# Kernel optimization log

Measured on AMD Instinct MI355X. Metric: run time of the kernel, lower is better.

## Reference

```python
import jax, jax.numpy as jnp
import numpy as np
import math

D_MODEL = 256
D_HEAD = 64
N_LEVELS = 2
N_HEADS = 8
N_POINTS = 4
SHAPES = [(100, 176), (50, 88)]  # (H, W) per level -> Len_in = 22000


def setup_inputs() -> dict:
    key = jax.random.key(0)
    ks = jax.random.split(key, 8)
    N, Lq = 2, 22000
    Len_in = sum(h * w for h, w in SHAPES)
    query = jax.random.normal(ks[0], (N, Lq, D_MODEL), jnp.float32)
    input_flatten = jax.random.normal(ks[1], (N, Len_in, D_MODEL), jnp.float32)
    input_spatial_shapes = jnp.array(SHAPES, jnp.int32)
    input_level_start_index = jnp.array([0, SHAPES[0][0] * SHAPES[0][1]], jnp.int32)
    # reference points in pixel units (original divides them by offset_normalizer)
    norm = jnp.array([[w, h] for (h, w) in SHAPES], jnp.float32)  # [L,2] as (x=W, y=H)
    reference_points = jax.random.uniform(ks[2], (N, Lq, N_LEVELS, 2), jnp.float32) * norm[None, None]
    xav = lambda k, shp: jax.random.normal(k, shp, jnp.float32) * math.sqrt(2.0 / (shp[0] + shp[1]))
    Wv = xav(ks[3], (D_MODEL, N_HEADS * D_HEAD))
    bv = jnp.zeros((N_HEADS * D_HEAD,), jnp.float32)
    Woff = jax.random.normal(ks[4], (D_MODEL, N_HEADS * N_LEVELS * N_POINTS * 2), jnp.float32) * 0.01
    # grid-init bias exactly as in _reset_parameters
    thetas = jnp.arange(N_HEADS, dtype=jnp.float32) * (2.0 * math.pi / N_HEADS)
    grid = jnp.stack([jnp.cos(thetas), jnp.sin(thetas)], -1)
    grid = grid / jnp.max(jnp.abs(grid), -1, keepdims=True)
    grid = jnp.tile(grid[:, None, None, :], (1, N_LEVELS, N_POINTS, 1))
    grid = grid * jnp.arange(1, N_POINTS + 1, dtype=jnp.float32)[None, None, :, None]
    boff = grid.reshape(-1)
    Wattn = jax.random.normal(ks[5], (D_MODEL, N_HEADS * N_LEVELS * N_POINTS), jnp.float32) * 0.01
    battn = jnp.zeros((N_HEADS * N_LEVELS * N_POINTS,), jnp.float32)
    Wo = xav(ks[6], (N_HEADS * D_HEAD, D_MODEL))
    bo = jnp.zeros((D_MODEL,), jnp.float32)
    return dict(query=query, reference_points=reference_points, input_flatten=input_flatten,
                Wv=Wv, bv=bv, Woff=Woff, boff=boff, Wattn=Wattn, battn=battn, Wo=Wo, bo=bo,
                input_spatial_shapes=input_spatial_shapes,
                input_level_start_index=input_level_start_index)


def ms_deform_core(value, sampling_locations, attention_weights, shapes_np):
    # value: [N, Len_in, H, D]; sampling_locations: [N, Lq, H, L, P, 2] in [0,1]
    # attention_weights: [N, Lq, H, L, P]
    N, _, Hh_, D = value.shape
    Lq = sampling_locations.shape[1]
    P = sampling_locations.shape[4]
    out = jnp.zeros((N, Lq, Hh_, D), value.dtype)
    start = 0
    for lvl, (Hl, Wl) in enumerate(shapes_np):
        Hl, Wl = int(Hl), int(Wl)
        v = value[:, start:start + Hl * Wl]  # [N, Hl*Wl, H, D]
        start += Hl * Wl
        loc = sampling_locations[:, :, :, lvl]  # [N, Lq, H, P, 2]
        # grid_sample align_corners=False convention
        x = loc[..., 0] * Wl - 0.5
        y = loc[..., 1] * Hl - 0.5
        x0 = jnp.floor(x); y0 = jnp.floor(y)
        fx = x - x0; fy = y - y0
        x0i = x0.astype(jnp.int32); y0i = y0.astype(jnp.int32)
        acc = jnp.zeros((N, Lq, P, Hh_, D), value.dtype)
        for dx, dy, w in ((0, 0, (1 - fx) * (1 - fy)), (1, 0, fx * (1 - fy)),
                          (0, 1, (1 - fx) * fy), (1, 1, fx * fy)):
            xi = x0i + dx; yi = y0i + dy
            valid = (xi >= 0) & (xi < Wl) & (yi >= 0) & (yi < Hl)
            idx = jnp.clip(yi, 0, Hl - 1) * Wl + jnp.clip(xi, 0, Wl - 1)  # [N, Lq, H, P]
            idx_t = idx.transpose(0, 1, 3, 2).reshape(N, Lq * P, Hh_, 1)
            g = jnp.take_along_axis(v, idx_t, axis=1).reshape(N, Lq, P, Hh_, D)
            wz = jnp.where(valid, w, 0.0)  # zero padding outside
            acc = acc + g * wz.transpose(0, 1, 3, 2)[..., None]
        out = out + jnp.einsum('nqphd,nqhp->nqhd', acc, attention_weights[:, :, :, lvl])
    return out.reshape(N, Lq, Hh_ * D)


def reference(query, reference_points, input_flatten, Wv, bv, Woff, boff, Wattn, battn, Wo, bo,
              input_spatial_shapes, input_level_start_index):
    shapes_np = np.asarray(input_spatial_shapes)
    N, Lq, _ = query.shape
    value = (input_flatten @ Wv + bv).reshape(N, -1, N_HEADS, D_HEAD)
    off = (query @ Woff + boff).reshape(N, Lq, N_HEADS, N_LEVELS, N_POINTS, 2)
    aw = jax.nn.softmax((query @ Wattn + battn).reshape(N, Lq, N_HEADS, N_LEVELS * N_POINTS), -1)
    aw = aw.reshape(N, Lq, N_HEADS, N_LEVELS, N_POINTS)
    normalizer = jnp.stack([shapes_np[:, 1], shapes_np[:, 0]], -1).astype(jnp.float32)  # [L,2] (W,H)
    loc = (reference_points[:, :, None, :, None, :] + off) / normalizer[None, None, None, :, None, :]
    out = ms_deform_core(value, loc, aw, shapes_np)
    return out @ Wo + bo
```

## Files before the change

kernel.cpp:

```cpp
#include <hip/hip_runtime.h>

#define LQ        22000
#define LEN_IN    22000
#define NB        2

typedef _Float16 half8 __attribute__((ext_vector_type(8)));
typedef _Float16 half4 __attribute__((ext_vector_type(4)));
typedef float    floatx4 __attribute__((ext_vector_type(4)));

__global__ __launch_bounds__(256) void prep_kernel(
    const float* __restrict__ Wv, const float* __restrict__ Woff,
    const float* __restrict__ Wattn, const float* __restrict__ Wo,
    const float* __restrict__ boff, const float* __restrict__ battn,
    _Float16* __restrict__ WvT, _Float16* __restrict__ WofT,
    _Float16* __restrict__ WoT, float* __restrict__ biascat)
{
    const int i = blockIdx.x * 256 + threadIdx.x;
    if (i < 131072) {
        int k = i >> 9, n = i & 511;
        WvT[n * 256 + k] = (_Float16)Wv[i];
    } else if (i < 163840) {
        int j = i - 131072; int k = j >> 7, n = j & 127;
        WofT[n * 256 + k] = (_Float16)Woff[j];
    } else if (i < 180224) {
        int j = i - 163840; int k = j >> 6, n = j & 63;
        WofT[(128 + n) * 256 + k] = (_Float16)Wattn[j];
    } else if (i < 311296) {
        int j = i - 180224; int k = j >> 8, n = j & 255;
        WoT[n * 512 + k] = (_Float16)Wo[j];
    } else if (i < 311488) {
        int j = i - 311296;
        biascat[j] = (j < 128) ? boff[j] : battn[j - 128];
    }
}

__global__ void f32_to_f16_kernel(const float* __restrict__ src,
                                  _Float16* __restrict__ dst, int n4)
{
    int i = blockIdx.x * blockDim.x + threadIdx.x;
    const int stride = gridDim.x * blockDim.x;
    for (; i < n4; i += stride) {
        float4 v = reinterpret_cast<const float4*>(src)[i];
        half4 h;
        h[0] = (_Float16)v.x; h[1] = (_Float16)v.y;
        h[2] = (_Float16)v.z; h[3] = (_Float16)v.w;
        reinterpret_cast<half4*>(dst)[i] = h;
    }
}

template<bool OUT_F16>
__global__ __launch_bounds__(256) void gemm_f16_kernel(
    const _Float16* __restrict__ A,
    const _Float16* __restrict__ BT,
    const float* __restrict__ bias,
    void* __restrict__ C,
    int M, int N, int K)
{
    __shared__ __align__(16) _Float16 sA[128][72];
    __shared__ __align__(16) _Float16 sB[64][72];

    const int t  = threadIdx.x;
    const int m0 = blockIdx.x * 128;
    const int n0 = blockIdx.y * 64;

    const int w    = t >> 6;
    const int lane = t & 63;
    const int wm   = w * 32;
    const int lrow = lane & 15;
    const int lk   = (lane >> 4) * 8;

    const int ar = t >> 1;
    const int ah = (t & 1) * 32;
    const int br = t >> 2;
    const int bs = (t & 3) * 16;

    floatx4 acc[2][4] = {};

    for (int k0 = 0; k0 < K; k0 += 64) {
        {
            int4 v0 = {0,0,0,0}, v1 = {0,0,0,0}, v2 = {0,0,0,0}, v3 = {0,0,0,0};
            const int arow = m0 + ar;
            if (arow < M) {
                const int4* src = reinterpret_cast<const int4*>(A + (size_t)arow * K + k0 + ah);
                v0 = src[0]; v1 = src[1]; v2 = src[2]; v3 = src[3];
            }
            int4* dst = reinterpret_cast<int4*>(&sA[ar][ah]);
            dst[0] = v0; dst[1] = v1; dst[2] = v2; dst[3] = v3;
        }
        {
            const int4* src = reinterpret_cast<const int4*>(BT + (size_t)(n0 + br) * K + k0 + bs);
            int4* dst = reinterpret_cast<int4*>(&sB[br][bs]);
            dst[0] = src[0]; dst[1] = src[1];
        }
        __syncthreads();

        #pragma unroll
        for (int kb = 0; kb < 2; ++kb) {
            const int ko = kb * 32 + lk;
            half8 a0 = *reinterpret_cast<const half8*>(&sA[wm + lrow][ko]);
            half8 a1 = *reinterpret_cast<const half8*>(&sA[wm + 16 + lrow][ko]);
            half8 b0 = *reinterpret_cast<const half8*>(&sB[lrow][ko]);
            half8 b1 = *reinterpret_cast<const half8*>(&sB[16 + lrow][ko]);
            half8 b2 = *reinterpret_cast<const half8*>(&sB[32 + lrow][ko]);
            half8 b3 = *reinterpret_cast<const half8*>(&sB[48 + lrow][ko]);
            acc[0][0] = __builtin_amdgcn_mfma_f32_16x16x32_f16(a0, b0, acc[0][0], 0, 0, 0);
            acc[0][1] = __builtin_amdgcn_mfma_f32_16x16x32_f16(a0, b1, acc[0][1], 0, 0, 0);
            acc[0][2] = __builtin_amdgcn_mfma_f32_16x16x32_f16(a0, b2, acc[0][2], 0, 0, 0);
            acc[0][3] = __builtin_amdgcn_mfma_f32_16x16x32_f16(a0, b3, acc[0][3], 0, 0, 0);
            acc[1][0] = __builtin_amdgcn_mfma_f32_16x16x32_f16(a1, b0, acc[1][0], 0, 0, 0);
            acc[1][1] = __builtin_amdgcn_mfma_f32_16x16x32_f16(a1, b1, acc[1][1], 0, 0, 0);
            acc[1][2] = __builtin_amdgcn_mfma_f32_16x16x32_f16(a1, b2, acc[1][2], 0, 0, 0);
            acc[1][3] = __builtin_amdgcn_mfma_f32_16x16x32_f16(a1, b3, acc[1][3], 0, 0, 0);
        }
        __syncthreads();
    }

    const int crow = (lane >> 4) * 4;
    const int ccol = lane & 15;
    #pragma unroll
    for (int fm = 0; fm < 2; ++fm) {
        #pragma unroll
        for (int fn = 0; fn < 4; ++fn) {
            const int col = n0 + fn * 16 + ccol;
            const float b = bias[col];
            #pragma unroll
            for (int r2 = 0; r2 < 4; ++r2) {
                const int row = m0 + wm + fm * 16 + crow + r2;
                if (row < M) {
                    const float val = acc[fm][fn][r2] + b;
                    if (OUT_F16)
                        ((_Float16*)C)[(size_t)row * N + col] = (_Float16)val;
                    else
                        ((float*)C)[(size_t)row * N + col] = val;
                }
            }
        }
    }
}

__global__ __launch_bounds__(256) void sampler_kernel(
    const _Float16* __restrict__ value,
    const _Float16* __restrict__ logits,
    const float*    __restrict__ refp,
    _Float16* __restrict__ sampled)
{
    const int t  = threadIdx.x;
    const int qh = t >> 7;
    const int q  = blockIdx.x * 2 + qh;
    const int tl = t & 127;

    __shared__ __align__(16) int4   s_idx[2][72];
    __shared__ __align__(16) float4 s_w[2][72];

    if (tl < 64) {
        const int s = tl;
        const int h = s >> 3;
        const int l = (s >> 2) & 1;
        const int p = s & 3;
        const _Float16* lg = logits + (size_t)q * 192;

        float logit[8];
        float m = -1e30f;
        #pragma unroll
        for (int j = 0; j < 8; ++j) {
            logit[j] = (float)lg[128 + h * 8 + j];
            m = fmaxf(m, logit[j]);
        }
        float den = 0.f;
        #pragma unroll
        for (int j = 0; j < 8; ++j) den += __expf(logit[j] - m);
        const float aw = __expf(logit[l * 4 + p] - m) / den;

        const int Hl = l ? 50 : 100;
        const int Wl = l ? 88 : 176;
        const int st = l ? 17600 : 0;
        const float rx = refp[q * 4 + l * 2 + 0];
        const float ry = refp[q * 4 + l * 2 + 1];
        const float ox = (float)lg[h * 16 + l * 8 + p * 2 + 0];
        const float oy = (float)lg[h * 16 + l * 8 + p * 2 + 1];

        const float x = rx + ox - 0.5f;
        const float y = ry + oy - 0.5f;
        const float x0f = floorf(x), y0f = floorf(y);
        const float fx = x - x0f, fy = y - y0f;
        const int x0 = (int)x0f, y0 = (int)y0f;

        int4  iv;
        float4 wv;
        #pragma unroll
        for (int c = 0; c < 4; ++c) {
            const int xi = x0 + (c & 1);
            const int yi = y0 + (c >> 1);
            const bool valid = (xi >= 0) & (xi < Wl) & (yi >= 0) & (yi < Hl);
            const float wb = ((c & 1) ? fx : 1.f - fx) * ((c >> 1) ? fy : 1.f - fy);
            const int xc = min(max(xi, 0), Wl - 1);
            const int yc = min(max(yi, 0), Hl - 1);
            iv[c] = st + yc * Wl + xc;
            wv[c] = valid ? wb * aw : 0.f;
        }
        const int slot = h * 9 + (l * 4 + p);
        s_idx[qh][slot] = iv;
        s_w[qh][slot]   = wv;
    }
    __syncthreads();

    const int h  = tl >> 4;
    const int d4 = (tl & 15) * 4;
    const _Float16* vbase = value + h * 64 + d4;

    float a0 = 0.f, a1 = 0.f, a2 = 0.f, a3 = 0.f;
    #pragma unroll
    for (int s8 = 0; s8 < 8; ++s8) {
        const int4   iv = s_idx[qh][h * 9 + s8];
        const float4 wv = s_w[qh][h * 9 + s8];
        #pragma unroll
        for (int c = 0; c < 4; ++c) {
            const half4 v = *reinterpret_cast<const half4*>(vbase + (size_t)iv[c] * 512);
            const float w = wv[c];
            a0 = fmaf(w, (float)v[0], a0);
            a1 = fmaf(w, (float)v[1], a1);
            a2 = fmaf(w, (float)v[2], a2);
            a3 = fmaf(w, (float)v[3], a3);
        }
    }
    half4 o;
    o[0] = (_Float16)a0; o[1] = (_Float16)a1;
    o[2] = (_Float16)a2; o[3] = (_Float16)a3;
    *reinterpret_cast<half4*>(sampled + (size_t)q * 512 + h * 64 + d4) = o;
}

extern "C" void kernel_launch(void* const* d_in, const int* in_sizes, int n_in,
                              void* d_out, int out_size, void* d_ws, size_t ws_size,
                              hipStream_t stream)
{
    const float* query  = (const float*)d_in[0];
    const float* refp   = (const float*)d_in[1];
    const float* inflat = (const float*)d_in[2];
    const float* Wv     = (const float*)d_in[3];
    const float* bv     = (const float*)d_in[4];
    const float* Woff   = (const float*)d_in[5];
    const float* boff   = (const float*)d_in[6];
    const float* Wattn  = (const float*)d_in[7];
    const float* battn  = (const float*)d_in[8];
    const float* Wo     = (const float*)d_in[9];
    const float* bo     = (const float*)d_in[10];
    float* out = (float*)d_out;

    char* ws = (char*)d_ws;
    size_t off = 0;
    auto take = [&](size_t bytes) { char* p = ws + off; off = (off + bytes + 255) & ~(size_t)255; return p; };
    _Float16* WvT     = (_Float16*)take(512 * 256 * 2);
    _Float16* WofT    = (_Float16*)take(192 * 256 * 2);
    _Float16* WoT     = (_Float16*)take(256 * 512 * 2);
    float*    biascat = (float*)   take(192 * 4);
    _Float16* inbf    = (_Float16*)take((size_t)LEN_IN * 256 * 2);
    _Float16* qbf     = (_Float16*)take((size_t)LQ * 256 * 2);
    _Float16* value   = (_Float16*)take((size_t)LEN_IN * 512 * 2);
    _Float16* logits  = (_Float16*)take((size_t)LQ * 192 * 2);
    _Float16* sampled = (_Float16*)take((size_t)LQ * 512 * 2);

    prep_kernel<<<(311488 + 255) / 256, 256, 0, stream>>>(
        Wv, Woff, Wattn, Wo, boff, battn, WvT, WofT, WoT, biascat);

    const int MGRID = (LQ + 127) / 128;

    for (int n = 0; n < NB; ++n) {
        const float* in_n  = inflat + (size_t)n * LEN_IN * 256;
        const float* q_n   = query  + (size_t)n * LQ * 256;
        const float* rp_n  = refp   + (size_t)n * LQ * 4;
        float*       out_n = out    + (size_t)n * LQ * 256;

        f32_to_f16_kernel<<<1024, 256, 0, stream>>>(in_n, inbf, LEN_IN * 256 / 4);
        f32_to_f16_kernel<<<1024, 256, 0, stream>>>(q_n, qbf, LQ * 256 / 4);

        gemm_f16_kernel<true><<<dim3(MGRID, 8), 256, 0, stream>>>(
            inbf, WvT, bv, value, LEN_IN, 512, 256);
        gemm_f16_kernel<true><<<dim3(MGRID, 3), 256, 0, stream>>>(
            qbf, WofT, biascat, logits, LQ, 192, 256);

        sampler_kernel<<<LQ / 2, 256, 0, stream>>>(value, logits, rp_n, sampled);

        gemm_f16_kernel<false><<<dim3(MGRID, 4), 256, 0, stream>>>(
            sampled, WoT, bo, out_n, LQ, 256, 512);
    }
}
```

Before: 384.3 us.

## Fuse f32-to-f16 conversion into GEMM loads, batch projections, use packed-half sampler

The value and offset/attention GEMMs now read fp32 inputs directly and convert to fp16 while staging into shared memory. This drops the separate conversion kernels and their round trip through memory, and each GEMM is launched once over both batches instead of per batch. The sampler is reorganised to one wavefront per query with 8 halves per lane, and it accumulates in packed fp16 math with fp16 weights. That cuts load instructions and FMA count but lowers accumulation precision.

```diff
diff --git a/kernel.cpp b/kernel.cpp
--- a/kernel.cpp
+++ b/kernel.cpp
@@ -6,6 +6,7 @@
 
 typedef _Float16 half8 __attribute__((ext_vector_type(8)));
 typedef _Float16 half4 __attribute__((ext_vector_type(4)));
+typedef _Float16 half2 __attribute__((ext_vector_type(2)));
 typedef float    floatx4 __attribute__((ext_vector_type(4)));
 
 __global__ __launch_bounds__(256) void prep_kernel(
@@ -34,23 +35,9 @@
     }
 }
 
-__global__ void f32_to_f16_kernel(const float* __restrict__ src,
-                                  _Float16* __restrict__ dst, int n4)
-{
-    int i = blockIdx.x * blockDim.x + threadIdx.x;
-    const int stride = gridDim.x * blockDim.x;
-    for (; i < n4; i += stride) {
-        float4 v = reinterpret_cast<const float4*>(src)[i];
-        half4 h;
-        h[0] = (_Float16)v.x; h[1] = (_Float16)v.y;
-        h[2] = (_Float16)v.z; h[3] = (_Float16)v.w;
-        reinterpret_cast<half4*>(dst)[i] = h;
-    }
-}
-
-template<bool OUT_F16>
-__global__ __launch_bounds__(256) void gemm_f16_kernel(
-    const _Float16* __restrict__ A,
+template<bool A_F32, bool OUT_F16>
+__global__ __launch_bounds__(256) void gemm_kernel(
+    const void* __restrict__ Aq,
     const _Float16* __restrict__ BT,
     const float* __restrict__ bias,
     void* __restrict__ C,
@@ -77,11 +64,25 @@
     floatx4 acc[2][4] = {};
 
     for (int k0 = 0; k0 < K; k0 += 64) {
-        {
-            int4 v0 = {0,0,0,0}, v1 = {0,0,0,0}, v2 = {0,0,0,0}, v3 = {0,0,0,0};
-            const int arow = m0 + ar;
+        const int arow = m0 + ar;
+        if constexpr (A_F32) {
+            const float4* src = reinterpret_cast<const float4*>(
+                (const float*)Aq + (size_t)arow * K + k0 + ah);
+            half4* dst = reinterpret_cast<half4*>(&sA[ar][ah]);
+            #pragma unroll
+            for (int j = 0; j < 8; ++j) {
+                float4 v = {0.f, 0.f, 0.f, 0.f};
+                if (arow < M) v = src[j];
+                half4 h;
+                h[0] = (_Float16)v.x; h[1] = (_Float16)v.y;
+                h[2] = (_Float16)v.z; h[3] = (_Float16)v.w;
+                dst[j] = h;
+            }
+        } else {
+            int4 v0 = {0,0,0,0}, v1 = v0, v2 = v0, v3 = v0;
             if (arow < M) {
-                const int4* src = reinterpret_cast<const int4*>(A + (size_t)arow * K + k0 + ah);
+                const int4* src = reinterpret_cast<const int4*>(
+                    (const _Float16*)Aq + (size_t)arow * K + k0 + ah);
                 v0 = src[0]; v1 = src[1]; v2 = src[2]; v3 = src[3];
             }
             int4* dst = reinterpret_cast<int4*>(&sA[ar][ah]);
@@ -144,16 +145,16 @@
     const float*    __restrict__ refp,
     _Float16* __restrict__ sampled)
 {
-    const int t  = threadIdx.x;
-    const int qh = t >> 7;
-    const int q  = blockIdx.x * 2 + qh;
-    const int tl = t & 127;
-
-    __shared__ __align__(16) int4   s_idx[2][72];
-    __shared__ __align__(16) float4 s_w[2][72];
-
-    if (tl < 64) {
-        const int s = tl;
+    const int t    = threadIdx.x;
+    const int wq   = t >> 6;
+    const int lane = t & 63;
+    const int q    = blockIdx.x * 4 + wq;
+
+    __shared__ __align__(16) int4  s_idx[4][72];
+    __shared__ __align__(16) uint4 s_w[4][72];
+
+    {
+        const int s = lane;
         const int h = s >> 3;
         const int l = (s >> 2) & 1;
         const int p = s & 3;
@@ -186,47 +187,57 @@
         const int x0 = (int)x0f, y0 = (int)y0f;
 
         int4  iv;
-        float4 wv;
+        uint4 wv;
         #pragma unroll
         for (int c = 0; c < 4; ++c) {
             const int xi = x0 + (c & 1);
             const int yi = y0 + (c >> 1);
             const bool valid = (xi >= 0) & (xi < Wl) & (yi >= 0) & (yi < Hl);
             const float wb = ((c & 1) ? fx : 1.f - fx) * ((c >> 1) ? fy : 1.f - fy);
+            const float wz = valid ? wb * aw : 0.f;
             const int xc = min(max(xi, 0), Wl - 1);
             const int yc = min(max(yi, 0), Hl - 1);
             iv[c] = st + yc * Wl + xc;
-            wv[c] = valid ? wb * aw : 0.f;
+            union { half2 h; unsigned int u; } cv;
+            cv.h[0] = (_Float16)wz; cv.h[1] = cv.h[0];
+            wv[c] = cv.u;
         }
         const int slot = h * 9 + (l * 4 + p);
-        s_idx[qh][slot] = iv;
-        s_w[qh][slot]   = wv;
+        s_idx[wq][slot] = iv;
+        s_w[wq][slot]   = wv;
     }
     __syncthreads();
 
-    const int h  = tl >> 4;
-    const int d4 = (tl & 15) * 4;
-    const _Float16* vbase = value + h * 64 + d4;
-
-    float a0 = 0.f, a1 = 0.f, a2 = 0.f, a3 = 0.f;
+    const int h  = lane >> 3;
+    const int d8 = (lane & 7) * 8;
+    const _Float16* vbase = value + h * 64 + d8;
+
+    half2 acc0 = {0.f16, 0.f16}, acc1 = acc0, acc2 = acc0, acc3 = acc0;
     #pragma unroll
     for (int s8 = 0; s8 < 8; ++s8) {
-        const int4   iv = s_idx[qh][h * 9 + s8];
-        const float4 wv = s_w[qh][h * 9 + s8];
+        const int4  iv = s_idx[wq][h * 9 + s8];
+        const uint4 wv = s_w[wq][h * 9 + s8];
         #pragma unroll
         for (int c = 0; c < 4; ++c) {
-            const half4 v = *reinterpret_cast<const half4*>(vbase + (size_t)iv[c] * 512);
-            const float w = wv[c];
-            a0 = fmaf(w, (float)v[0], a0);
-            a1 = fmaf(w, (float)v[1], a1);
-            a2 = fmaf(w, (float)v[2], a2);
-            a3 = fmaf(w, (float)v[3], a3);
-        }
-    }
-    half4 o;
-    o[0] = (_Float16)a0; o[1] = (_Float16)a1;
-    o[2] = (_Float16)a2; o[3] = (_Float16)a3;
-    *reinterpret_cast<half4*>(sampled + (size_t)q * 512 + h * 64 + d4) = o;
+            const half8 v = *reinterpret_cast<const half8*>(vbase + (size_t)iv[c] * 512);
+            union { unsigned int u; half2 h; } cv; cv.u = wv[c];
+            const half2 wh = cv.h;
+            half2 p0; p0[0] = v[0]; p0[1] = v[1];
+            half2 p1; p1[0] = v[2]; p1[1] = v[3];
+            half2 p2; p2[0] = v[4]; p2[1] = v[5];
+            half2 p3; p3[0] = v[6]; p3[1] = v[7];
+            acc0 += p0 * wh;
+            acc1 += p1 * wh;
+            acc2 += p2 * wh;
+            acc3 += p3 * wh;
+        }
+    }
+    half8 o;
+    o[0] = acc0[0]; o[1] = acc0[1];
+    o[2] = acc1[0]; o[3] = acc1[1];
+    o[4] = acc2[0]; o[5] = acc2[1];
+    o[6] = acc3[0]; o[7] = acc3[1];
+    *reinterpret_cast<half8*>(sampled + (size_t)q * 512 + h * 64 + d8) = o;
 }
 
 extern "C" void kernel_launch(void* const* d_in, const int* in_sizes, int n_in,
@@ -253,34 +264,29 @@
     _Float16* WofT    = (_Float16*)take(192 * 256 * 2);
     _Float16* WoT     = (_Float16*)take(256 * 512 * 2);
     float*    biascat = (float*)   take(192 * 4);
-    _Float16* inbf    = (_Float16*)take((size_t)LEN_IN * 256 * 2);
-    _Float16* qbf     = (_Float16*)take((size_t)LQ * 256 * 2);
-    _Float16* value   = (_Float16*)take((size_t)LEN_IN * 512 * 2);
-    _Float16* logits  = (_Float16*)take((size_t)LQ * 192 * 2);
+    _Float16* value   = (_Float16*)take((size_t)NB * LEN_IN * 512 * 2);
+    _Float16* logits  = (_Float16*)take((size_t)NB * LQ * 192 * 2);
     _Float16* sampled = (_Float16*)take((size_t)LQ * 512 * 2);
 
     prep_kernel<<<(311488 + 255) / 256, 256, 0, stream>>>(
         Wv, Woff, Wattn, Wo, boff, battn, WvT, WofT, WoT, biascat);
 
-    const int MGRID = (LQ + 127) / 128;
+    const int M2   = NB * LQ;
+    const int MG2  = (M2 + 127) / 128;
+    const int MG1  = (LQ + 127) / 128;
+
+    gemm_kernel<true, true><<<dim3(MG2, 8), 256, 0, stream>>>(
+        inflat, WvT, bv, value, M2, 512, 256);
+    gemm_kernel<true, true><<<dim3(MG2, 3), 256, 0, stream>>>(
+        query, WofT, biascat, logits, M2, 192, 256);
 
     for (int n = 0; n < NB; ++n) {
-        const float* in_n  = inflat + (size_t)n * LEN_IN * 256;
-        const float* q_n   = query  + (size_t)n * LQ * 256;
-        const float* rp_n  = refp   + (size_t)n * LQ * 4;
-        float*       out_n = out    + (size_t)n * LQ * 256;
-
-        f32_to_f16_kernel<<<1024, 256, 0, stream>>>(in_n, inbf, LEN_IN * 256 / 4);
-        f32_to_f16_kernel<<<1024, 256, 0, stream>>>(q_n, qbf, LQ * 256 / 4);
-
-        gemm_f16_kernel<true><<<dim3(MGRID, 8), 256, 0, stream>>>(
-            inbf, WvT, bv, value, LEN_IN, 512, 256);
-        gemm_f16_kernel<true><<<dim3(MGRID, 3), 256, 0, stream>>>(
-            qbf, WofT, biascat, logits, LQ, 192, 256);
-
-        sampler_kernel<<<LQ / 2, 256, 0, stream>>>(value, logits, rp_n, sampled);
-
-        gemm_f16_kernel<false><<<dim3(MGRID, 4), 256, 0, stream>>>(
-            sampled, WoT, bo, out_n, LQ, 256, 512);
-    }
-}
+        sampler_kernel<<<LQ / 4, 256, 0, stream>>>(
+            value  + (size_t)n * LEN_IN * 512,
+            logits + (size_t)n * LQ * 192,
+            refp   + (size_t)n * LQ * 4,
+            sampled);
+        gemm_kernel<false, false><<<dim3(MG1, 4), 256, 0, stream>>>(
+            sampled, WoT, bo, out + (size_t)n * LQ * 256, LQ, 256, 512);
+    }
+}
```

New measurement: 395.6 us. 1.03x slower.
